# Optimization experiments

Hardware: AMD Instinct MI355X
Metric: run time of the kernel (lower is better)

Reference implementation:

```python
import jax, jax.numpy as jnp
import numpy as np

B, C, T = 64, 64, 4096
SFREQ = 256.0
NYQ = SFREQ / 2.0
NF = 2            # n_filters = len(filter_f_mean)
NOUT = 4
F_BINS = T // 2 + 1
N_FEAT = NF * C * (C - 1) // 2


def setup_inputs() -> dict:
    key = jax.random.key(0)
    kx, kw = jax.random.split(key)
    x = jax.random.normal(kx, (B, C, T), dtype=jnp.float32)
    # learned filter params (normalized exactly as in __init__)
    f_mean = jnp.full((NF,), 23.0 / NYQ, dtype=jnp.float32)
    bandwidth = jnp.full((NF,), 44.0 / NYQ, dtype=jnp.float32)
    shape_p = jnp.full((NF,), 2.0, dtype=jnp.float32)
    group_delay = jnp.full((NF,), 20.0 / 1000.0, dtype=jnp.float32)
    lin_w = jax.random.normal(kw, (NOUT, N_FEAT), dtype=jnp.float32) / np.sqrt(N_FEAT)
    lin_b = jnp.zeros((NOUT,), dtype=jnp.float32)
    return dict(x=x, f_mean=f_mean, bandwidth=bandwidth, shape_p=shape_p,
                group_delay=group_delay, lin_w=lin_w, lin_b=lin_b)


def _construct_filters(f_mean, bandwidth, shape_p, group_delay):
    # normalized frequency grid: fftfreq[:T//2] ++ [nyquist], / nyquist
    freqs = np.fft.fftfreq(T, d=1.0 / SFREQ)[: T // 2]
    n_range = jnp.asarray(np.concatenate([freqs, [NYQ]]) / NYQ, dtype=jnp.float32)  # (F,)
    fm = jnp.clip(f_mean, 1.0 / NYQ, 45.0 / NYQ)[:, None]        # (NF,1)
    bw = jnp.clip(bandwidth, 1.0 / NYQ, 1.0)[:, None]
    p = (jnp.clip(shape_p, 2.0, 3.0) * 8.0 - 14.0)[:, None]      # shape*8-14
    log2 = jnp.log(jnp.float32(2.0))
    scale = bw / (2.0 * log2 ** (1.0 / p))
    mag = jnp.exp(-(((jnp.abs(n_range[None, :] - fm)) + 1e-8) / scale) ** p)  # (NF,F)
    mag = mag / jnp.max(mag, axis=-1, keepdims=True)
    phase = jnp.linspace(0.0, SFREQ, F_BINS, dtype=jnp.float32)
    pha = -group_delay[:, None] * phase[None, :] * jnp.pi
    return mag * jnp.cos(pha), mag * jnp.sin(pha)  # (NF,F) each


def _eegminer_plv(x, f_mean, bandwidth, shape_p, group_delay, lin_w, lin_b):
    filt_re, filt_im = _construct_filters(f_mean, bandwidth, shape_p, group_delay)
    X = jnp.fft.rfft(x, axis=-1)  # (B,C,F) complex
    # NOTE: torch multiplies the view_as_real tensor by the (real, imag) filter
    # stack COMPONENT-WISE (not a complex multiply); reproduce that faithfully.
    re = X.real[:, :, None, :] * filt_re[None, None]  # (B,C,NF,F)
    im = X.imag[:, :, None, :] * filt_im[None, None]
    re = jnp.transpose(re, (0, 2, 1, 3))  # (B,NF,C,F)
    im = jnp.transpose(im, (0, 2, 1, 3))
    # hilbert_freq(forward_fourier=False): double all bins, halve DC, zero-pad to T
    dc_scale = jnp.where(jnp.arange(F_BINS) == 0, 1.0, 2.0).astype(x.dtype)
    pad = ((0, 0), (0, 0), (0, 0), (0, T - F_BINS))  # T - F = F - 2
    z = jnp.pad(re * dc_scale, pad) + 1j * jnp.pad(im * dc_scale, pad)
    analytic = jnp.fft.ifft(z, axis=-1)  # (B,NF,C,T) complex
    amp = jnp.sqrt(analytic.real ** 2 + analytic.imag ** 2 + 1e-6)
    ur = analytic.real / amp
    ui = analytic.imag / amp
    rr = jnp.einsum('bfct,bfdt->bfcd', ur, ur)
    ii = jnp.einsum('bfct,bfdt->bfcd', ui, ui)
    ri = jnp.einsum('bfct,bfdt->bfcd', ur, ui)
    ir = jnp.einsum('bfct,bfdt->bfcd', ui, ur)
    corr_re = rr + ii
    corr_im = ri - ir
    plv = jnp.sqrt(corr_re ** 2 + corr_im ** 2 + 1e-6) / T  # (B,NF,C,C)
    plv = jnp.transpose(plv, (0, 2, 3, 1))  # (B,C,C,NF)
    iu, ju = np.triu_indices(C, 1)
    feats = plv[:, iu, ju, :].reshape(x.shape[0], N_FEAT)
    # BatchNorm1d(affine=False), training mode: batch stats, biased var, eps=1e-5
    mu = jnp.mean(feats, axis=0)
    var = jnp.mean((feats - mu) ** 2, axis=0)
    feats = (feats - mu) / jnp.sqrt(var + 1e-5)
    return feats @ lin_w.T + lin_b


def reference(x, f_mean, bandwidth, shape_p, group_delay, lin_w, lin_b):
    return _eegminer_plv(x, f_mean, bandwidth, shape_p, group_delay, lin_w, lin_b)
```

## Files before the change

kernel.cpp:

```cpp
#include <hip/hip_runtime.h>
#include <math.h>

#define T_N     4096
#define B_N     64
#define C_N     64
#define NFILT   2
#define F_BINS  2049
#define NPAIRS  2016
#define NFEAT   4032
#define NOUT    4
#define TSG     4
#define NKS     32
#define XSLOTS  2304

#define PI_F 3.14159265358979323846f

typedef _Float16 f16x8 __attribute__((ext_vector_type(8)));
typedef _Float16 f16x2 __attribute__((ext_vector_type(2)));
typedef float    f32x4 __attribute__((ext_vector_type(4)));
typedef float    cplx  __attribute__((ext_vector_type(2)));


#define OFF_U     65536
#define G_BYTES   (128 * TSG * 12288 * 4)

__global__ __launch_bounds__(256) void filter_kernel(
    const float* __restrict__ fm_, const float* __restrict__ bw_,
    const float* __restrict__ sp_, const float* __restrict__ gd_,
    cplx* __restrict__ filt) {
  __shared__ float smag[F_BINS];
  __shared__ float sred[256];
  const int tid = threadIdx.x;
  const int f = blockIdx.x;
  cplx* Fc = filt + f * 4096;
  for (int p = tid; p < 4096; p += 256) Fc[p] = cplx{0.0f, 0.0f};
  const float fm = fminf(fmaxf(fm_[f], 1.0f / 128.0f), 45.0f / 128.0f);
  const float bw = fminf(fmaxf(bw_[f], 1.0f / 128.0f), 1.0f);
  const float pp = fminf(fmaxf(sp_[f], 2.0f), 3.0f) * 8.0f - 14.0f;
  const float gd = gd_[f];
  const float scale = bw / (2.0f * powf(0.69314718055994531f, 1.0f / pp));
  float lmax = 0.0f;
  for (int i = tid; i < F_BINS; i += 256) {
    const float n = (float)i / 2048.0f;
    const float m = expf(-powf((fabsf(n - fm) + 1e-8f) / scale, pp));
    smag[i] = m;
    lmax = fmaxf(lmax, m);
  }
  sred[tid] = lmax;
  __syncthreads();
  for (int s = 128; s > 0; s >>= 1) {
    if (tid < s) sred[tid] = fmaxf(sred[tid], sred[tid + s]);
    __syncthreads();
  }
  const float inv = 1.0f / sred[0];
  for (int k = tid; k < F_BINS; k += 256) {
    const float m = smag[k] * inv;
    const float pha = -gd * ((float)k * 0.125f) * PI_F;
    float sn, cs;
    sincosf(pha, &sn, &cs);
    const float dcs = (k == 0) ? 1.0f : 2.0f;
    const float sT = dcs * (1.0f / (float)T_N);
    const int p = (k & 0xF00) + ((k & 15) << 4) + ((k >> 4) & 15);
    Fc[p] = cplx{m * cs * sT, m * sn * sT};
  }
}

__device__ __forceinline__ cplx cmul(cplx a, cplx w) {
  const cplx wx = __builtin_shufflevector(w, w, 0, 0);
  const cplx wy = __builtin_shufflevector(w, w, 1, 1);
  const cplx as = __builtin_shufflevector(a, a, 1, 0);
  return cplx{-as.x, as.y} * wy + a * wx;
}
__device__ __forceinline__ cplx twid(float rev) {
  return cplx{__builtin_amdgcn_cosf(rev), __builtin_amdgcn_sinf(rev)};
}

template<int SGN>
__device__ __forceinline__ void dft16(cplx* __restrict__ v) {
  const float sg = (float)SGN;
  const float C1 = 0.923879532511287f, S1 = 0.382683432365090f;
  const float Hh = 0.707106781186548f;
  cplx g[16];
#pragma unroll
  for (int n2 = 0; n2 < 4; ++n2) {
    const cplx a = v[n2], b = v[4 + n2], c = v[8 + n2], d = v[12 + n2];
    const cplx t0 = a + c, t1 = a - c, t2 = b + d, t3 = b - d;
    const cplx it3 = (SGN < 0) ? cplx{t3.y, -t3.x} : cplx{-t3.y, t3.x};
    g[n2]      = t0 + t2;
    g[8 + n2]  = t0 - t2;
    g[4 + n2]  = t1 + it3;
    g[12 + n2] = t1 - it3;
  }
  g[5]  = cmul(g[5],  cplx{C1,  sg * S1});
  g[6]  = cmul(g[6],  cplx{Hh,  sg * Hh});
  g[7]  = cmul(g[7],  cplx{S1,  sg * C1});
  g[9]  = cmul(g[9],  cplx{Hh,  sg * Hh});
  g[10] = (SGN < 0) ? cplx{g[10].y, -g[10].x} : cplx{-g[10].y, g[10].x};
  g[11] = cmul(g[11], cplx{-Hh, sg * Hh});
  g[13] = cmul(g[13], cplx{S1,  sg * C1});
  g[14] = cmul(g[14], cplx{-Hh, sg * Hh});
  g[15] = cmul(g[15], cplx{-C1, -sg * S1});
#pragma unroll
  for (int k1 = 0; k1 < 4; ++k1) {
    const cplx a = g[4 * k1], b = g[4 * k1 + 1];
    const cplx c = g[4 * k1 + 2], d = g[4 * k1 + 3];
    const cplx t0 = a + c, t1 = a - c, t2 = b + d, t3 = b - d;
    const cplx it3 = (SGN < 0) ? cplx{t3.y, -t3.x} : cplx{-t3.y, t3.x};
    v[k1]      = t0 + t2;
    v[8 + k1]  = t0 - t2;
    v[4 + k1]  = t1 + it3;
    v[12 + k1] = t1 - it3;
  }
}

__device__ __forceinline__ void tr_group_half(cplx* __restrict__ v,
                                              cplx* __restrict__ hlds, int t) {
  const int g = t >> 4, j1 = t & 15;
  const int rowb = (g & 7) * 264;
  if (g < 8) {
#pragma unroll
    for (int r = 0; r < 16; ++r)
      hlds[rowb + r * 16 + ((j1 + r) & 15)] = v[r];
  }
  __syncthreads();
  if (g < 8) {
#pragma unroll
    for (int a = 0; a < 16; ++a)
      v[a] = hlds[rowb + j1 * 16 + ((a + j1) & 15)];
  }
  __syncthreads();
  if (g >= 8) {
#pragma unroll
    for (int r = 0; r < 16; ++r)
      hlds[rowb + r * 16 + ((j1 + r) & 15)] = v[r];
  }
  __syncthreads();
  if (g >= 8) {
#pragma unroll
    for (int a = 0; a < 16; ++a)
      v[a] = hlds[rowb + j1 * 16 + ((a + j1) & 15)];
  }
}

__global__ __launch_bounds__(256) void fwd_kernel(
    const float* __restrict__ x, f16x2* __restrict__ Xs, int chunkbase) {
  const int cp = blockIdx.x & 31;
  const int bb = blockIdx.x >> 5;
  const int b  = chunkbase + bb;
  const int t  = threadIdx.x;
  const int j1 = t & 15;
  const int g  = t >> 4;
  __shared__ cplx hlds[8 * 264];
  __shared__ cplx TB[256];

  TB[t] = twid(-(float)(g * j1) * (1.0f / 256.0f));

  cplx v[16];
  const float* xp0 = x + ((size_t)(b * C_N + 2 * cp)) * T_N;
  const float* xp1 = xp0 + T_N;
#pragma unroll
  for (int r = 0; r < 16; ++r)
    v[r] = cplx{xp0[r * 256 + t], xp1[r * 256 + t]};

  dft16<-1>(v);
#pragma unroll
  for (int k = 1; k < 16; ++k)
    v[k] = cmul(v[k], twid((float)(t * k) * (-1.0f / 4096.0f)));

  {
    __syncthreads();
#pragma unroll
    for (int k = 0; k < 8; ++k) hlds[k * 264 + t] = v[k];
    __syncthreads();
    cplx tmp[8];
    if (g < 8) {
      const int base = g * 264 + j1;
#pragma unroll
      for (int m = 0; m < 8; ++m) tmp[m] = hlds[base + (8 + m) * 16];
#pragma unroll
      for (int m = 0; m < 8; ++m) v[m] = hlds[base + m * 16];
    }
    __syncthreads();
#pragma unroll
    for (int k = 0; k < 8; ++k) hlds[k * 264 + t] = v[8 + k];
    __syncthreads();
    if (g < 8) {
#pragma unroll
      for (int m = 0; m < 8; ++m) v[8 + m] = tmp[m];
    } else {
      const int base = (g - 8) * 264 + j1;
#pragma unroll
      for (int m = 0; m < 16; ++m) v[m] = hlds[base + m * 16];
    }
  }

  dft16<-1>(v);
#pragma unroll
  for (int k = 1; k < 16; ++k)
    v[k] = cmul(v[k], TB[k * 16 + j1]);

  __syncthreads();
  tr_group_half(v, hlds, t);
  dft16<-1>(v);

  const int k1 = g;
  const int tp = (k1 == 0) ? ((16 - j1) & 15)
                           : (((16 - k1) << 4) | (15 - j1));
  f16x2* Xp0 = Xs + (size_t)(bb * C_N + 2 * cp) * XSLOTS;
  f16x2* Xp1 = Xp0 + XSLOTS;

  __syncthreads();
#pragma unroll
  for (int q = 8; q < 16; ++q) hlds[(q - 8) * 264 + t] = v[q];
  __syncthreads();
#pragma unroll
  for (int q = 0; q < 8; ++q) {
    const int qp = (t == 0) ? ((16 - q) & 15) : (15 - q);
    const cplx Z  = v[q];
    const cplx Zp = (qp >= 8) ? hlds[(qp - 8) * 264 + tp] : Z;
    f16x2 h0, h1;
    h0[0] = (_Float16)(0.5f * (Z.x + Zp.x));
    h0[1] = (_Float16)(0.5f * (Z.y - Zp.y));
    h1[0] = (_Float16)(0.5f * (Z.y + Zp.y));
    h1[1] = (_Float16)(0.5f * (Zp.x - Z.x));
    Xp0[q * 256 + t] = h0;
    Xp1[q * 256 + t] = h1;
  }
  __syncthreads();
#pragma unroll
  for (int q = 0; q < 8; ++q) hlds[q * 264 + t] = v[q];
  __syncthreads();
  {
    const cplx Z  = v[8];
    const cplx Zp = (t == 0) ? Z : hlds[7 * 264 + tp];
    f16x2 h0, h1;
    h0[0] = (_Float16)(0.5f * (Z.x + Zp.x));
    h0[1] = (_Float16)(0.5f * (Z.y - Zp.y));
    h1[0] = (_Float16)(0.5f * (Z.y + Zp.y));
    h1[1] = (_Float16)(0.5f * (Zp.x - Z.x));
    Xp0[8 * 256 + t] = h0;
    Xp1[8 * 256 + t] = h1;
  }
}

__global__ __launch_bounds__(256) void inv_kernel(
    const f16x2* __restrict__ Xs, const cplx* __restrict__ filt,
    _Float16* __restrict__ Urg, _Float16* __restrict__ Uig) {
  const int f  = blockIdx.x & 1;
  const int c  = (blockIdx.x >> 1) & 63;
  const int bb = blockIdx.x >> 7;
  const int t  = threadIdx.x;
  const int j1 = t & 15;
  const int g  = t >> 4;
  __shared__ cplx hlds[8 * 264];
  __shared__ cplx TB[256];
  __shared__ cplx TCB[256];

  {
    const int prod = g * j1;
    TB[t]  = twid((float)prod * (1.0f / 256.0f));
    TCB[t] = twid((float)prod * (1.0f / 4096.0f));
  }

  cplx v[16];
  const f16x2* Xp = Xs + (size_t)(bb * C_N + c) * XSLOTS;
  const cplx* Fc = filt + f * 4096;
#pragma unroll
  for (int q = 0; q < 9; ++q) {
    const f16x2 xv = Xp[q * 256 + t];
    v[q] = cplx{(float)xv[0], (float)xv[1]} * Fc[q * 256 + t];
  }
#pragma unroll
  for (int q = 9; q < 16; ++q)
    v[q] = cplx{0.0f, 0.0f};

  __syncthreads();

  dft16<1>(v);
#pragma unroll
  for (int k = 1; k < 16; ++k)
    v[k] = cmul(v[k], TB[k * 16 + j1]);

  tr_group_half(v, hlds, t);

  dft16<1>(v);
  {
    const cplx tcb = TCB[t];
    v[0] = cmul(v[0], tcb);
#pragma unroll
    for (int m1 = 1; m1 < 16; ++m1) {
      const cplx w = cmul(tcb, TB[m1 * 16 + g]);
      v[m1] = cmul(v[m1], w);
    }
  }

  {
    cplx tmp[8];
    const int base = (g & 7) * 264 + j1;
    __syncthreads();
    if (g < 8) {
#pragma unroll
      for (int m = 0; m < 16; ++m) hlds[base + m * 16] = v[m];
    }
    __syncthreads();
#pragma unroll
    for (int k = 0; k < 8; ++k) tmp[k] = hlds[k * 264 + t];
    __syncthreads();
    if (g >= 8) {
#pragma unroll
      for (int m = 0; m < 16; ++m) hlds[base + m * 16] = v[m];
    }
    __syncthreads();
#pragma unroll
    for (int k = 0; k < 8; ++k) v[8 + k] = hlds[k * 264 + t];
#pragma unroll
    for (int k = 0; k < 8; ++k) v[k] = tmp[k];
  }

  dft16<1>(v);

  const int sl = bb * 2 + f;
  _Float16* upr = Urg + ((size_t)sl * C_N + c) * T_N;
  _Float16* upi = Uig + ((size_t)sl * C_N + c) * T_N;
#pragma unroll
  for (int n1 = 0; n1 < 16; ++n1) {
    const float ir = rsqrtf(v[n1].x * v[n1].x + v[n1].y * v[n1].y + 1e-6f);
    upr[n1 * 256 + t] = (_Float16)(v[n1].x * ir);
    upi[n1 * 256 + t] = (_Float16)(v[n1].y * ir);
  }
}

__global__ __launch_bounds__(256) void gram_kernel(
    const _Float16* __restrict__ Urg, const _Float16* __restrict__ Uig,
    float* __restrict__ Gp, int slicebase) {
  const int sl = blockIdx.x / TSG;
  const int ts = blockIdx.x % TSG;
  const int tid = threadIdx.x;
  const int w = tid >> 6;
  const int lane = tid & 63;
  __shared__ _Float16 sUr[2][64 * 40], sUi[2][64 * 40];

  const int row = tid >> 2, quarter = tid & 3;
  const size_t goff = (size_t)sl * C_N * T_N + (size_t)row * T_N
                      + ts * (T_N / TSG) + quarter * 8;
  const int loff = row * 40 + quarter * 8;
  const int frow = (lane & 15) * 40 + (lane >> 4) * 8;
  const int aoff = w * 640 + frow;

  f32x4 accRr[4] = {}, accIi[4] = {}, accRi[4] = {};

  f16x8 rr = *(const f16x8*)&Urg[goff];
  f16x8 ri = *(const f16x8*)&Uig[goff];
  int cur = 0;
  for (int ks = 0; ks < NKS; ++ks) {
    *(f16x8*)&sUr[cur][loff] = rr;
    *(f16x8*)&sUi[cur][loff] = ri;
    if (ks + 1 < NKS) {
      rr = *(const f16x8*)&Urg[goff + (ks + 1) * 32];
      ri = *(const f16x8*)&Uig[goff + (ks + 1) * 32];
    }
    __syncthreads();
    const f16x8 ar = *(const f16x8*)&sUr[cur][aoff];
    const f16x8 ai = *(const f16x8*)&sUi[cur][aoff];
#pragma unroll
    for (int n = 0; n < 4; ++n) {
      const f16x8 br = *(const f16x8*)&sUr[cur][n * 640 + frow];
      const f16x8 bi = *(const f16x8*)&sUi[cur][n * 640 + frow];
      accRr[n] = __builtin_amdgcn_mfma_f32_16x16x32_f16(ar, br, accRr[n], 0, 0, 0);
      accIi[n] = __builtin_amdgcn_mfma_f32_16x16x32_f16(ai, bi, accIi[n], 0, 0, 0);
      accRi[n] = __builtin_amdgcn_mfma_f32_16x16x32_f16(ar, bi, accRi[n], 0, 0, 0);
    }
    cur ^= 1;
  }

  float* Gs = Gp + (size_t)((slicebase + sl) * TSG + ts) * 12288;
  const int r0 = w * 16 + (lane >> 4) * 4;
  const int c0 = lane & 15;
#pragma unroll
  for (int n = 0; n < 4; ++n) {
    const bool upper = (n >= w);
#pragma unroll
    for (int e = 0; e < 4; ++e) {
      const int idx = (r0 + e) * 64 + n * 16 + c0;
      if (upper) {
        Gs[idx] = accRr[n][e];
        Gs[4096 + idx] = accIi[n][e];
      }
      Gs[8192 + idx] = accRi[n][e];
    }
  }
}

__global__ __launch_bounds__(256) void plv_kernel(
    const float* __restrict__ Gp, float* __restrict__ feats) {
  const int idx = blockIdx.x * 256 + threadIdx.x;
  if (idx >= B_N * NFILT * NPAIRS) return;
  const int slice = idx / NPAIRS;
  const int p = idx - slice * NPAIRS;
  const int b = slice >> 1, f = slice & 1;
  const int r = NPAIRS - 1 - p;
  int m = (int)((sqrtf((float)(8 * r + 1)) - 1.0f) * 0.5f);
  while ((m + 1) * (m + 2) / 2 <= r) ++m;
  while (m * (m + 1) / 2 > r) --m;
  const int c = 62 - m;
  const int d = 63 - (r - m * (m + 1) / 2);
  const float* Gs = Gp + (size_t)slice * TSG * 12288;
  float rr = 0, ii = 0, ri = 0, ir = 0;
#pragma unroll
  for (int ts = 0; ts < TSG; ++ts) {
    const float* P = Gs + ts * 12288;
    rr += P[c * 64 + d];
    ii += P[4096 + c * 64 + d];
    ri += P[8192 + c * 64 + d];
    ir += P[8192 + d * 64 + c];
  }
  const float cre = rr + ii;
  const float cim = ri - ir;
  const float plv = sqrtf(cre * cre + cim * cim + 1e-6f) * (1.0f / (float)T_N);
  feats[b * NFEAT + p * NFILT + f] = plv;
}

__global__ __launch_bounds__(64) void stats_kernel(
    const float* __restrict__ feats, float* __restrict__ stats) {
  const int j = blockIdx.x * 64 + threadIdx.x;
  if (j >= NFEAT) return;
  float s = 0.0f;
  for (int b = 0; b < B_N; ++b) s += feats[b * NFEAT + j];
  const float mu = s * (1.0f / (float)B_N);
  float v = 0.0f;
  for (int b = 0; b < B_N; ++b) {
    const float d = feats[b * NFEAT + j] - mu;
    v += d * d;
  }
  v *= (1.0f / (float)B_N);
  stats[j] = mu;
  stats[NFEAT + j] = 1.0f / sqrtf(v + 1e-5f);
}

__global__ __launch_bounds__(256) void out_kernel(
    const float* __restrict__ feats, const float* __restrict__ stats,
    const float* __restrict__ w, const float* __restrict__ lb,
    float* __restrict__ out) {
  const int b = blockIdx.x;
  const int tid = threadIdx.x;
  float acc0 = 0, acc1 = 0, acc2 = 0, acc3 = 0;
  for (int j = tid; j < NFEAT; j += 256) {
    const float v = (feats[b * NFEAT + j] - stats[j]) * stats[NFEAT + j];
    acc0 += v * w[0 * NFEAT + j];
    acc1 += v * w[1 * NFEAT + j];
    acc2 += v * w[2 * NFEAT + j];
    acc3 += v * w[3 * NFEAT + j];
  }
  __shared__ float red[4][256];
  red[0][tid] = acc0; red[1][tid] = acc1; red[2][tid] = acc2; red[3][tid] = acc3;
  __syncthreads();
  for (int s = 128; s > 0; s >>= 1) {
    if (tid < s) {
#pragma unroll
      for (int o = 0; o < 4; ++o) red[o][tid] += red[o][tid + s];
    }
    __syncthreads();
  }
  if (tid < 4) out[b * NOUT + tid] = red[tid][0] + lb[tid];
}

extern "C" void kernel_launch(void* const* d_in, const int* in_sizes, int n_in,
                              void* d_out, int out_size, void* d_ws, size_t ws_size,
                              hipStream_t stream) {
  const float* x  = (const float*)d_in[0];
  const float* fm = (const float*)d_in[1];
  const float* bw = (const float*)d_in[2];
  const float* sp = (const float*)d_in[3];
  const float* gd = (const float*)d_in[4];
  const float* lw = (const float*)d_in[5];
  const float* lb = (const float*)d_in[6];
  float* out = (float*)d_out;
  char* base = (char*)d_ws;

  const size_t perCB = 2 * 1048576 + (size_t)C_N * XSLOTS * 4;
  const size_t fixed = OFF_U + (size_t)G_BYTES + (size_t)B_N * NFEAT * 4 + 2 * NFEAT * 4;
  int CB = 64;
  if (ws_size < fixed + (size_t)64 * perCB) CB = 32;
  if (ws_size < fixed + (size_t)32 * perCB) CB = 16;
  const int nchunk = B_N / CB;

  const size_t u_bytes = (size_t)CB * 1048576;
  const size_t x_bytes = (size_t)CB * C_N * XSLOTS * 4;
  cplx*     filt  = (cplx*)base;
  _Float16* Urg   = (_Float16*)(base + OFF_U);
  _Float16* Uig   = (_Float16*)(base + OFF_U + u_bytes);
  f16x2*    Xs    = (f16x2*)(base + OFF_U + 2 * u_bytes);
  float*    Gp    = (float*)(base + OFF_U + 2 * u_bytes + x_bytes);
  float*    feats = (float*)(base + OFF_U + 2 * u_bytes + x_bytes + G_BYTES);
  float*    stats = feats + (size_t)B_N * NFEAT;

  filter_kernel<<<NFILT, 256, 0, stream>>>(fm, bw, sp, gd, filt);

  for (int chunk = 0; chunk < nchunk; ++chunk) {
    fwd_kernel<<<CB * (C_N / 2), 256, 0, stream>>>(x, Xs, chunk * CB);
    inv_kernel<<<CB * C_N * NFILT, 256, 0, stream>>>(Xs, filt, Urg, Uig);
    gram_kernel<<<CB * 2 * TSG, 256, 0, stream>>>(Urg, Uig, Gp, chunk * CB * 2);
  }

  plv_kernel<<<(B_N * NFILT * NPAIRS + 255) / 256, 256, 0, stream>>>(Gp, feats);
  stats_kernel<<<(NFEAT + 63) / 64, 64, 0, stream>>>(feats, stats);
  out_kernel<<<B_N, 256, 0, stream>>>(feats, stats, lw, lb, out);
}
```

Baseline: 136.4 us.

## Fuse forward FFT and filtered inverse FFTs into one kernel

Merges the forward rFFT kernel and the per-filter inverse FFT kernel into a single fused kernel. The spectrum stays in registers in fp32 rather than passing through an fp16 global buffer, and each block runs four inverse transforms (2 channels x 2 filters) serially. The intent is to remove the global write and read of the spectrum, one kernel launch per chunk, and some workspace. In exchange the grid shrinks to a quarter of the blocks, each doing more serial work, which may hurt occupancy and latency hiding. Register pressure also rises from holding X0/X1.

```diff
diff --git a/kernel.cpp b/kernel.cpp
--- a/kernel.cpp
+++ b/kernel.cpp
@@ -11,7 +11,6 @@
 #define NOUT    4
 #define TSG     4
 #define NKS     32
-#define XSLOTS  2304
 
 #define PI_F 3.14159265358979323846f
 
@@ -71,6 +70,12 @@
   const cplx as = __builtin_shufflevector(a, a, 1, 0);
   return cplx{-as.x, as.y} * wy + a * wx;
 }
+__device__ __forceinline__ cplx cmulc(cplx a, cplx w) {
+  const cplx wx = __builtin_shufflevector(w, w, 0, 0);
+  const cplx wy = __builtin_shufflevector(w, w, 1, 1);
+  const cplx as = __builtin_shufflevector(a, a, 1, 0);
+  return cplx{as.x, -as.y} * wy + a * wx;
+}
 __device__ __forceinline__ cplx twid(float rev) {
   return cplx{__builtin_amdgcn_cosf(rev), __builtin_amdgcn_sinf(rev)};
 }
@@ -142,8 +147,77 @@
   }
 }
 
-__global__ __launch_bounds__(256) void fwd_kernel(
-    const float* __restrict__ x, f16x2* __restrict__ Xs, int chunkbase) {
+__device__ __forceinline__ void inv_body(
+    const cplx* __restrict__ X, const cplx* __restrict__ Fc,
+    cplx* __restrict__ hlds, const cplx* __restrict__ TB,
+    const cplx* __restrict__ TCB,
+    _Float16* __restrict__ upr, _Float16* __restrict__ upi, int t) {
+  const int j1 = t & 15;
+  const int g  = t >> 4;
+  __syncthreads();
+
+  cplx v[16];
+#pragma unroll
+  for (int q = 0; q < 9; ++q)
+    v[q] = X[q] * Fc[q * 256 + t];
+#pragma unroll
+  for (int q = 9; q < 16; ++q)
+    v[q] = cplx{0.0f, 0.0f};
+
+  dft16<1>(v);
+#pragma unroll
+  for (int k = 1; k < 16; ++k)
+    v[k] = cmul(v[k], TB[k * 16 + j1]);
+
+  tr_group_half(v, hlds, t);
+
+  dft16<1>(v);
+  {
+    const cplx tcb = TCB[t];
+    v[0] = cmul(v[0], tcb);
+#pragma unroll
+    for (int m1 = 1; m1 < 16; ++m1) {
+      const cplx w = cmul(tcb, TB[m1 * 16 + g]);
+      v[m1] = cmul(v[m1], w);
+    }
+  }
+
+  {
+    cplx tmp[8];
+    const int base = (g & 7) * 264 + j1;
+    __syncthreads();
+    if (g < 8) {
+#pragma unroll
+      for (int m = 0; m < 16; ++m) hlds[base + m * 16] = v[m];
+    }
+    __syncthreads();
+#pragma unroll
+    for (int k = 0; k < 8; ++k) tmp[k] = hlds[k * 264 + t];
+    __syncthreads();
+    if (g >= 8) {
+#pragma unroll
+      for (int m = 0; m < 16; ++m) hlds[base + m * 16] = v[m];
+    }
+    __syncthreads();
+#pragma unroll
+    for (int k = 0; k < 8; ++k) v[8 + k] = hlds[k * 264 + t];
+#pragma unroll
+    for (int k = 0; k < 8; ++k) v[k] = tmp[k];
+  }
+
+  dft16<1>(v);
+
+#pragma unroll
+  for (int n1 = 0; n1 < 16; ++n1) {
+    const float ir = rsqrtf(v[n1].x * v[n1].x + v[n1].y * v[n1].y + 1e-6f);
+    upr[n1 * 256 + t] = (_Float16)(v[n1].x * ir);
+    upi[n1 * 256 + t] = (_Float16)(v[n1].y * ir);
+  }
+}
+
+__global__ __launch_bounds__(256) void fused_kernel(
+    const float* __restrict__ x, const cplx* __restrict__ filt,
+    _Float16* __restrict__ Urg, _Float16* __restrict__ Uig, int chunkbase) {
   const int cp = blockIdx.x & 31;
   const int bb = blockIdx.x >> 5;
   const int b  = chunkbase + bb;
@@ -152,8 +226,13 @@
   const int g  = t >> 4;
   __shared__ cplx hlds[8 * 264];
   __shared__ cplx TB[256];
-
-  TB[t] = twid(-(float)(g * j1) * (1.0f / 256.0f));
+  __shared__ cplx TCB[256];
+
+  {
+    const int prod = g * j1;
+    TB[t]  = twid((float)prod * (1.0f / 256.0f));
+    TCB[t] = twid((float)prod * (1.0f / 4096.0f));
+  }
 
   cplx v[16];
   const float* xp0 = x + ((size_t)(b * C_N + 2 * cp)) * T_N;
@@ -197,17 +276,15 @@
   dft16<-1>(v);
 #pragma unroll
   for (int k = 1; k < 16; ++k)
-    v[k] = cmul(v[k], TB[k * 16 + j1]);
+    v[k] = cmulc(v[k], TB[k * 16 + j1]);
 
   __syncthreads();
   tr_group_half(v, hlds, t);
   dft16<-1>(v);
 
-  const int k1 = g;
-  const int tp = (k1 == 0) ? ((16 - j1) & 15)
-                           : (((16 - k1) << 4) | (15 - j1));
-  f16x2* Xp0 = Xs + (size_t)(bb * C_N + 2 * cp) * XSLOTS;
-  f16x2* Xp1 = Xp0 + XSLOTS;
+  const int tp = (g == 0) ? ((16 - j1) & 15)
+                          : (((16 - g) << 4) | (15 - j1));
+  cplx X0[9], X1[9];
 
   __syncthreads();
 #pragma unroll
@@ -218,13 +295,8 @@
     const int qp = (t == 0) ? ((16 - q) & 15) : (15 - q);
     const cplx Z  = v[q];
     const cplx Zp = (qp >= 8) ? hlds[(qp - 8) * 264 + tp] : Z;
-    f16x2 h0, h1;
-    h0[0] = (_Float16)(0.5f * (Z.x + Zp.x));
-    h0[1] = (_Float16)(0.5f * (Z.y - Zp.y));
-    h1[0] = (_Float16)(0.5f * (Z.y + Zp.y));
-    h1[1] = (_Float16)(0.5f * (Zp.x - Z.x));
-    Xp0[q * 256 + t] = h0;
-    Xp1[q * 256 + t] = h1;
+    X0[q] = cplx{0.5f * (Z.x + Zp.x), 0.5f * (Z.y - Zp.y)};
+    X1[q] = cplx{0.5f * (Z.y + Zp.y), 0.5f * (Zp.x - Z.x)};
   }
   __syncthreads();
 #pragma unroll
@@ -233,100 +305,21 @@
   {
     const cplx Z  = v[8];
     const cplx Zp = (t == 0) ? Z : hlds[7 * 264 + tp];
-    f16x2 h0, h1;
-    h0[0] = (_Float16)(0.5f * (Z.x + Zp.x));
-    h0[1] = (_Float16)(0.5f * (Z.y - Zp.y));
-    h1[0] = (_Float16)(0.5f * (Z.y + Zp.y));
-    h1[1] = (_Float16)(0.5f * (Zp.x - Z.x));
-    Xp0[8 * 256 + t] = h0;
-    Xp1[8 * 256 + t] = h1;
-  }
-}
-
-__global__ __launch_bounds__(256) void inv_kernel(
-    const f16x2* __restrict__ Xs, const cplx* __restrict__ filt,
-    _Float16* __restrict__ Urg, _Float16* __restrict__ Uig) {
-  const int f  = blockIdx.x & 1;
-  const int c  = (blockIdx.x >> 1) & 63;
-  const int bb = blockIdx.x >> 7;
-  const int t  = threadIdx.x;
-  const int j1 = t & 15;
-  const int g  = t >> 4;
-  __shared__ cplx hlds[8 * 264];
-  __shared__ cplx TB[256];
-  __shared__ cplx TCB[256];
-
-  {
-    const int prod = g * j1;
-    TB[t]  = twid((float)prod * (1.0f / 256.0f));
-    TCB[t] = twid((float)prod * (1.0f / 4096.0f));
-  }
-
-  cplx v[16];
-  const f16x2* Xp = Xs + (size_t)(bb * C_N + c) * XSLOTS;
-  const cplx* Fc = filt + f * 4096;
-#pragma unroll
-  for (int q = 0; q < 9; ++q) {
-    const f16x2 xv = Xp[q * 256 + t];
-    v[q] = cplx{(float)xv[0], (float)xv[1]} * Fc[q * 256 + t];
-  }
-#pragma unroll
-  for (int q = 9; q < 16; ++q)
-    v[q] = cplx{0.0f, 0.0f};
-
-  __syncthreads();
-
-  dft16<1>(v);
-#pragma unroll
-  for (int k = 1; k < 16; ++k)
-    v[k] = cmul(v[k], TB[k * 16 + j1]);
-
-  tr_group_half(v, hlds, t);
-
-  dft16<1>(v);
-  {
-    const cplx tcb = TCB[t];
-    v[0] = cmul(v[0], tcb);
-#pragma unroll
-    for (int m1 = 1; m1 < 16; ++m1) {
-      const cplx w = cmul(tcb, TB[m1 * 16 + g]);
-      v[m1] = cmul(v[m1], w);
-    }
-  }
-
-  {
-    cplx tmp[8];
-    const int base = (g & 7) * 264 + j1;
-    __syncthreads();
-    if (g < 8) {
-#pragma unroll
-      for (int m = 0; m < 16; ++m) hlds[base + m * 16] = v[m];
-    }
-    __syncthreads();
-#pragma unroll
-    for (int k = 0; k < 8; ++k) tmp[k] = hlds[k * 264 + t];
-    __syncthreads();
-    if (g >= 8) {
-#pragma unroll
-      for (int m = 0; m < 16; ++m) hlds[base + m * 16] = v[m];
-    }
-    __syncthreads();
-#pragma unroll
-    for (int k = 0; k < 8; ++k) v[8 + k] = hlds[k * 264 + t];
-#pragma unroll
-    for (int k = 0; k < 8; ++k) v[k] = tmp[k];
-  }
-
-  dft16<1>(v);
-
-  const int sl = bb * 2 + f;
-  _Float16* upr = Urg + ((size_t)sl * C_N + c) * T_N;
-  _Float16* upi = Uig + ((size_t)sl * C_N + c) * T_N;
-#pragma unroll
-  for (int n1 = 0; n1 < 16; ++n1) {
-    const float ir = rsqrtf(v[n1].x * v[n1].x + v[n1].y * v[n1].y + 1e-6f);
-    upr[n1 * 256 + t] = (_Float16)(v[n1].x * ir);
-    upi[n1 * 256 + t] = (_Float16)(v[n1].y * ir);
+    X0[8] = cplx{0.5f * (Z.x + Zp.x), 0.5f * (Z.y - Zp.y)};
+    X1[8] = cplx{0.5f * (Z.y + Zp.y), 0.5f * (Zp.x - Z.x)};
+  }
+
+  const int c0 = 2 * cp, c1 = 2 * cp + 1;
+#pragma unroll 1
+  for (int f = 0; f < NFILT; ++f) {
+    const cplx* Fc = filt + f * 4096;
+    const int sl = bb * 2 + f;
+    _Float16* upr0 = Urg + ((size_t)sl * C_N + c0) * T_N;
+    _Float16* upi0 = Uig + ((size_t)sl * C_N + c0) * T_N;
+    inv_body(X0, Fc, hlds, TB, TCB, upr0, upi0, t);
+    _Float16* upr1 = Urg + ((size_t)sl * C_N + c1) * T_N;
+    _Float16* upi1 = Uig + ((size_t)sl * C_N + c1) * T_N;
+    inv_body(X1, Fc, hlds, TB, TCB, upr1, upi1, t);
   }
 }
 
@@ -477,7 +470,7 @@
   float* out = (float*)d_out;
   char* base = (char*)d_ws;
 
-  const size_t perCB = 2 * 1048576 + (size_t)C_N * XSLOTS * 4;
+  const size_t perCB = 2 * 1048576;
   const size_t fixed = OFF_U + (size_t)G_BYTES + (size_t)B_N * NFEAT * 4 + 2 * NFEAT * 4;
   int CB = 64;
   if (ws_size < fixed + (size_t)64 * perCB) CB = 32;
@@ -485,20 +478,17 @@
   const int nchunk = B_N / CB;
 
   const size_t u_bytes = (size_t)CB * 1048576;
-  const size_t x_bytes = (size_t)CB * C_N * XSLOTS * 4;
   cplx*     filt  = (cplx*)base;
   _Float16* Urg   = (_Float16*)(base + OFF_U);
   _Float16* Uig   = (_Float16*)(base + OFF_U + u_bytes);
-  f16x2*    Xs    = (f16x2*)(base + OFF_U + 2 * u_bytes);
-  float*    Gp    = (float*)(base + OFF_U + 2 * u_bytes + x_bytes);
-  float*    feats = (float*)(base + OFF_U + 2 * u_bytes + x_bytes + G_BYTES);
+  float*    Gp    = (float*)(base + OFF_U + 2 * u_bytes);
+  float*    feats = (float*)(base + OFF_U + 2 * u_bytes + G_BYTES);
   float*    stats = feats + (size_t)B_N * NFEAT;
 
   filter_kernel<<<NFILT, 256, 0, stream>>>(fm, bw, sp, gd, filt);
 
   for (int chunk = 0; chunk < nchunk; ++chunk) {
-    fwd_kernel<<<CB * (C_N / 2), 256, 0, stream>>>(x, Xs, chunk * CB);
-    inv_kernel<<<CB * C_N * NFILT, 256, 0, stream>>>(Xs, filt, Urg, Uig);
+    fused_kernel<<<CB * (C_N / 2), 256, 0, stream>>>(x, filt, Urg, Uig, chunk * CB);
     gram_kernel<<<CB * 2 * TSG, 256, 0, stream>>>(Urg, Uig, Gp, chunk * CB * 2);
   }
 
```

Result: no change. 134.7 us (-1.3%).
